# Optimization experiments

Measured on AMD Instinct MI355X. Metric: run time of the kernel, lower is better.

## Reference

```python
import jax, jax.numpy as jnp
import numpy as np

ALPHA = 1.0

def setup_inputs() -> dict:
    key = jax.random.key(0)
    kx, kd = jax.random.split(key)
    B, L, D = 64, 256, 512
    x = jax.random.normal(kx, (B, L, D), dtype=jnp.float32)
    duration = jax.random.randint(kd, (B, L), 0, 8, dtype=jnp.int32)
    max_length = 1792  # L * max_duration
    return {"x": x, "duration": duration, "max_length": max_length}

def reference(x, duration, max_length):
    B, L, D = x.shape
    # round(duration * alpha) -> integer durations
    d = jnp.round(duration.astype(jnp.float32) * ALPHA).astype(jnp.int32)
    # rows with all-zero durations get one frame (original picks a random
    # position; we deterministically use position 0)
    row_sum = d.sum(axis=1)  # [B]
    d = jnp.where((row_sum == 0)[:, None] & (jnp.arange(L) == 0)[None, :], 1, d)
    # cumulative end offsets per phoneme: cum[b, j] = sum_{k<=j} d[b, k]
    cum = jnp.cumsum(d, axis=1)  # [B, L]
    t = jnp.arange(max_length)   # [T]
    # output frame t belongs to phoneme j where cum[j-1] <= t < cum[j]
    idx = jax.vmap(lambda c: jnp.searchsorted(c, t, side='right'))(cum)  # [B, T]
    idx = jnp.clip(idx, 0, L - 1)
    out = jnp.take_along_axis(x, idx[:, :, None], axis=1)  # [B, T, D]
    # zero-pad beyond each sequence's total length
    mask = (t[None, :] < cum[:, -1:]).astype(x.dtype)  # [B, T]
    out = out * mask[:, :, None]
    return out, max_length
```

## Files before the change

kernel.cpp:

```cpp
#include <hip/hip_runtime.h>


#define BB 64
#define LL 256
#define DD 512
#define TT 1792
#define D4 (DD / 4)

__global__ __launch_bounds__(256) void length_regulator_kernel(
    const float4* __restrict__ x4,
    const int*    __restrict__ dur,
    const int*    __restrict__ maxlen,
    float*        __restrict__ out)
{
    __shared__ int cum[LL];
    const int tid = threadIdx.x;
    const int b   = blockIdx.y;

    cum[tid] = dur[b * LL + tid];
    __syncthreads();
    #pragma unroll
    for (int off = 1; off < LL; off <<= 1) {
        int v = (tid >= off) ? cum[tid - off] : 0;
        __syncthreads();
        cum[tid] += v;
        __syncthreads();
    }
    int total = cum[LL - 1];
    if (total == 0) cum[tid] = 1;
    __syncthreads();
    total = cum[LL - 1];

    float4* out4 = (float4*)out;
    const int group  = tid >> 7;
    const int lane   = tid & 127;
    const int t_base = blockIdx.x * 16;

    #pragma unroll
    for (int j = 0; j < 8; ++j) {
        const int t = t_base + j * 2 + group;
        float4 val = make_float4(0.f, 0.f, 0.f, 0.f);
        if (t < total) {
            int lo = 0, hi = LL;
            while (lo < hi) {
                const int mid = (lo + hi) >> 1;
                if (cum[mid] <= t) lo = mid + 1; else hi = mid;
            }
            const int idx = (lo < LL - 1) ? lo : (LL - 1);
            val = x4[((size_t)b * LL + idx) * D4 + lane];
        }
        out4[((size_t)b * TT + t) * D4 + lane] = val;
    }

    if (b == 0 && blockIdx.x == 0 && tid == 0) {
        out[(size_t)BB * TT * DD] = (float)maxlen[0];
    }
}

extern "C" void kernel_launch(void* const* d_in, const int* in_sizes, int n_in,
                              void* d_out, int out_size, void* d_ws, size_t ws_size,
                              hipStream_t stream) {
    const float4* x4  = (const float4*)d_in[0];
    const int*    dur = (const int*)d_in[1];
    const int*    ml  = (const int*)d_in[2];
    float*        out = (float*)d_out;

    dim3 grid(TT / 16, BB);
    length_regulator_kernel<<<grid, dim3(256), 0, stream>>>(x4, dur, ml, out);
}
```

Baseline: 270.4 us.

## Replace per-frame binary search with shared index scatter over larger tiles

Each phoneme thread now writes its own index into a shared per-tile frame-to-phoneme map, which replaces the binary search done per output frame. Tiles grow from 16 to 64 frames, so each block's prefix sum over durations is amortized over more output rows and fewer blocks are launched. Output stores use nontemporal hints to avoid polluting the cache. This adds extra shared memory and a scatter loop with divergence, and the smaller grid means less parallelism.

```diff
diff --git a/kernel.cpp b/kernel.cpp
--- a/kernel.cpp
+++ b/kernel.cpp
@@ -6,18 +6,25 @@
 #define DD 512
 #define TT 1792
 #define D4 (DD / 4)
+#define TILE 64
+#define NBT (TT / TILE)
+
+typedef float f32x4 __attribute__((ext_vector_type(4)));
 
 __global__ __launch_bounds__(256) void length_regulator_kernel(
-    const float4* __restrict__ x4,
-    const int*    __restrict__ dur,
-    const int*    __restrict__ maxlen,
-    float*        __restrict__ out)
+    const f32x4* __restrict__ x4,
+    const int*   __restrict__ dur,
+    const int*   __restrict__ maxlen,
+    float*       __restrict__ out)
 {
     __shared__ int cum[LL];
+    __shared__ int idx_s[TILE];
     const int tid = threadIdx.x;
     const int b   = blockIdx.y;
+    const int t0  = blockIdx.x * TILE;
 
     cum[tid] = dur[b * LL + tid];
+    if (tid < TILE) idx_s[tid] = -1;
     __syncthreads();
     #pragma unroll
     for (int off = 1; off < LL; off <<= 1) {
@@ -29,27 +36,29 @@
     int total = cum[LL - 1];
     if (total == 0) cum[tid] = 1;
     __syncthreads();
-    total = cum[LL - 1];
 
-    float4* out4 = (float4*)out;
-    const int group  = tid >> 7;
-    const int lane   = tid & 127;
-    const int t_base = blockIdx.x * 16;
+    {
+        const int end   = cum[tid];
+        const int start = (tid > 0) ? cum[tid - 1] : 0;
+        const int lo = max(start, t0);
+        const int hi = min(end, t0 + TILE);
+        for (int t = lo; t < hi; ++t) idx_s[t - t0] = tid;
+    }
+    __syncthreads();
+
+    f32x4* out4 = (f32x4*)out;
+    const int group = tid >> 7;
+    const int lane  = tid & 127;
+    const f32x4 z   = (f32x4)(0.f);
 
     #pragma unroll
-    for (int j = 0; j < 8; ++j) {
-        const int t = t_base + j * 2 + group;
-        float4 val = make_float4(0.f, 0.f, 0.f, 0.f);
-        if (t < total) {
-            int lo = 0, hi = LL;
-            while (lo < hi) {
-                const int mid = (lo + hi) >> 1;
-                if (cum[mid] <= t) lo = mid + 1; else hi = mid;
-            }
-            const int idx = (lo < LL - 1) ? lo : (LL - 1);
-            val = x4[((size_t)b * LL + idx) * D4 + lane];
-        }
-        out4[((size_t)b * TT + t) * D4 + lane] = val;
+    for (int it = 0; it < TILE / 2; ++it) {
+        const int toff = it * 2 + group;
+        const int id   = idx_s[toff];
+        f32x4 v = z;
+        if (id >= 0)
+            v = x4[((size_t)b * LL + id) * D4 + lane];
+        __builtin_nontemporal_store(v, &out4[((size_t)b * TT + t0 + toff) * D4 + lane]);
     }
 
     if (b == 0 && blockIdx.x == 0 && tid == 0) {
@@ -60,11 +69,11 @@
 extern "C" void kernel_launch(void* const* d_in, const int* in_sizes, int n_in,
                               void* d_out, int out_size, void* d_ws, size_t ws_size,
                               hipStream_t stream) {
-    const float4* x4  = (const float4*)d_in[0];
-    const int*    dur = (const int*)d_in[1];
-    const int*    ml  = (const int*)d_in[2];
-    float*        out = (float*)d_out;
+    const f32x4* x4  = (const f32x4*)d_in[0];
+    const int*   dur = (const int*)d_in[1];
+    const int*   ml  = (const int*)d_in[2];
+    float*       out = (float*)d_out;
 
-    dim3 grid(TT / 16, BB);
+    dim3 grid(NBT, BB);
     length_regulator_kernel<<<grid, dim3(256), 0, stream>>>(x4, dur, ml, out);
 }
```

Result: no change. 271.8 us (+0.5%).
